# Performance work log

Measured on AMD Instinct MI355X. Metric: run time of the kernel, lower is better.

## Reference

```python
import jax, jax.numpy as jnp
import numpy as np
import math

D_MODEL = 1024
NHEAD = 16
D_HEAD = D_MODEL // NHEAD
TAU = 300.0
DELTA = 5.0 * 60.0  # delta_minutes -> seconds


def setup_inputs() -> dict:
    key = jax.random.key(0)
    ks = jax.random.split(key, 10)
    B, M = 4, 2048
    H = jax.random.normal(ks[0], (B, M, D_MODEL), dtype=jnp.float32)
    patch_mask = jax.random.randint(ks[1], (B, M), 0, 2).astype(jnp.int32)
    s = 1.0 / math.sqrt(D_MODEL)
    Wq = jax.random.normal(ks[2], (D_MODEL, D_MODEL), dtype=jnp.float32) * s
    bq = jnp.zeros((D_MODEL,), dtype=jnp.float32)
    Wk = jax.random.normal(ks[3], (D_MODEL, D_MODEL), dtype=jnp.float32) * s
    bk = jnp.zeros((D_MODEL,), dtype=jnp.float32)
    Wv = jax.random.normal(ks[4], (D_MODEL, D_MODEL), dtype=jnp.float32) * s
    bv = jnp.zeros((D_MODEL,), dtype=jnp.float32)
    Wo = jax.random.normal(ks[5], (D_MODEL, D_MODEL), dtype=jnp.float32) * s
    bo = jnp.zeros((D_MODEL,), dtype=jnp.float32)
    return {"H": H, "patch_mask": patch_mask, "Wq": Wq, "bq": bq,
            "Wk": Wk, "bk": bk, "Wv": Wv, "bv": bv, "Wo": Wo, "bo": bo}


def _time_bias(M):
    idx = jnp.arange(M)
    dist = jnp.abs(idx[:, None] - idx[None, :]).astype(jnp.float32) * DELTA
    w = jnp.exp(-dist / max(TAU, 1e-6))
    return jnp.log(w + 1e-12)  # (M, M)


def reference(H, patch_mask, Wq, bq, Wk, bk, Wv, bv, Wo, bo):
    B, M, D = H.shape
    nh, dh = NHEAD, D_HEAD
    # projections -> (B, nh, M, dh)
    q = (H @ Wq.T + bq).reshape(B, M, nh, dh).transpose(0, 2, 1, 3)
    k = (H @ Wk.T + bk).reshape(B, M, nh, dh).transpose(0, 2, 1, 3)
    v = (H @ Wv.T + bv).reshape(B, M, nh, dh).transpose(0, 2, 1, 3)
    attn = jnp.einsum('bhqd,bhkd->bhqk', q, k) / math.sqrt(dh)
    attn = attn + _time_bias(M)[None, None, :, :]
    key_pad = patch_mask <= 0  # (B, M)
    attn = jnp.where(key_pad[:, None, None, :], -1e9, attn)
    A = jax.nn.softmax(attn, axis=-1)
    out = jnp.einsum('bhqk,bhkd->bhqd', A, v)
    out = out.transpose(0, 2, 1, 3).reshape(B, M, D)
    out = out @ Wo.T + bo
    out = out * patch_mask[:, :, None].astype(out.dtype)
    return out
```

## Files before the change

kernel.cpp:

```cpp
#include <hip/hip_runtime.h>
#include <stdint.h>

typedef short short8 __attribute__((ext_vector_type(8)));
typedef float f32x4 __attribute__((ext_vector_type(4)));

#define B_    4
#define M_    2048
#define D_    1024
#define NH_   16
#define DH_   64
#define LOG2E 1.44269504f

__device__ __forceinline__ short f2bf(float f) {
  union { float f; uint32_t u; } v; v.f = f;
  uint32_t r = (v.u + 0x7fffu + ((v.u >> 16) & 1u)) >> 16;
  return (short)r;
}

__device__ __forceinline__ void gl_lds16(const void* g, void* l) {
  __builtin_amdgcn_global_load_lds(
      (__attribute__((address_space(1))) void*)(g),
      (__attribute__((address_space(3))) void*)(l),
      16, 0, 0);
}

__device__ __forceinline__ f32x4 mfma16(short8 a, short8 b, f32x4 c) {
  return __builtin_amdgcn_mfma_f32_16x16x32_bf16(a, b, c, 0, 0, 0);
}

__global__ __launch_bounds__(256) void cvt_all(const float* __restrict__ H,
                                               const float* __restrict__ s0,
                                               const float* __restrict__ s1,
                                               const float* __restrict__ s2,
                                               const float* __restrict__ s3,
                                               short* __restrict__ dH,
                                               short* __restrict__ d0,
                                               short* __restrict__ d1,
                                               short* __restrict__ d2,
                                               short* __restrict__ d3) {
  const int bidx = blockIdx.x;
  const float* src;
  short* dst;
  int i;
  if (bidx < 8192) {
    src = H; dst = dH; i = bidx * 256 + threadIdx.x;
  } else {
    const int y = (bidx - 8192) >> 10;
    src = (y == 0) ? s0 : (y == 1) ? s1 : (y == 2) ? s2 : s3;
    dst = (y == 0) ? d0 : (y == 1) ? d1 : (y == 2) ? d2 : d3;
    i = ((bidx - 8192) & 1023) * 256 + threadIdx.x;
  }
  float4 v = ((const float4*)src)[i];
  short4 o;
  o.x = f2bf(v.x); o.y = f2bf(v.y); o.z = f2bf(v.z); o.w = f2bf(v.w);
  ((short4*)dst)[i] = o;
}

__global__ __launch_bounds__(256, 3) void gemm_qkv(const short* __restrict__ A,
                                                   const short* __restrict__ Wqb,
                                                   const short* __restrict__ Wkb,
                                                   const short* __restrict__ Wvb,
                                                   const float* __restrict__ bq,
                                                   const float* __restrict__ bk,
                                                   const float* __restrict__ bv,
                                                   short* __restrict__ Qo,
                                                   short* __restrict__ Ko,
                                                   short* __restrict__ Vo) {
  __shared__ char smem_raw[34816];
  short* Abuf = (short*)smem_raw;
  short* Bbuf = (short*)smem_raw + 4096;

  const int L = blockIdx.x + 8 * (blockIdx.y + 64 * blockIdx.z);
  const int xcd = L & 7;
  const int s = L >> 3;
  const int m_local = s & 7;
  const int nz = s >> 3;
  const int nt = nz & 7, z = nz >> 3;
  const int m0 = (xcd * 8 + m_local) * 128;
  const int n0 = nt * 128;

  const short* Bt = (z == 0) ? Wqb : (z == 1) ? Wkb : Wvb;
  const float* bias = (z == 0) ? bq : (z == 1) ? bk : bv;
  const float scale = (z == 0) ? 0.125f : 1.0f;

  const int tid = threadIdx.x;
  const int w = tid >> 6, l = tid & 63;
  const int q4 = l >> 4, c = l & 15;
  const int wr = w >> 1, wc = w & 1;

  f32x4 acc[4][4] = {};
  const int arow = (l >> 2);
  const int acol = (l & 3) * 8;

  for (int kk = 0; kk < 32; ++kk) {
    const int k0 = kk * 32;
#pragma unroll
    for (int st = 0; st < 2; ++st) {
      const int chunk = w * 2 + st;
      gl_lds16(A + (size_t)(m0 + chunk * 16 + arow) * 1024 + k0 + acol,
               Abuf + chunk * 512);
      gl_lds16(Bt + (size_t)(n0 + chunk * 16 + arow) * 1024 + k0 + acol,
               Bbuf + chunk * 512);
    }
    __syncthreads();
    short8 af[4], bfr[4];
#pragma unroll
    for (int i = 0; i < 4; ++i)
      af[i] = *(const short8*)(Abuf + (wr * 64 + i * 16 + c) * 32 + q4 * 8);
#pragma unroll
    for (int j = 0; j < 4; ++j)
      bfr[j] = *(const short8*)(Bbuf + (wc * 64 + j * 16 + c) * 32 + q4 * 8);
#pragma unroll
    for (int i = 0; i < 4; ++i)
#pragma unroll
      for (int j = 0; j < 4; ++j)
        acc[i][j] = mfma16(af[i], bfr[j], acc[i][j]);
    __syncthreads();
  }

  if (z < 2) {
    short* Cb = (short*)smem_raw;
    short* out = (z == 0) ? Qo : Ko;
#pragma unroll
    for (int j = 0; j < 4; ++j) {
      const float bvv = bias[n0 + wc * 64 + j * 16 + c];
#pragma unroll
      for (int i = 0; i < 4; ++i)
#pragma unroll
        for (int r = 0; r < 4; ++r)
          Cb[(wr * 64 + i * 16 + q4 * 4 + r) * 136 + wc * 64 + j * 16 + c] =
              f2bf((acc[i][j][r] + bvv) * scale);
    }
    __syncthreads();
#pragma unroll
    for (int p = 0; p < 8; ++p) {
      const int g = p * 256 + tid;
      const int row = g >> 4, seg = g & 15;
      *(short8*)(out + (size_t)(m0 + row) * 1024 + n0 + seg * 8) =
          *(const short8*)(Cb + row * 136 + seg * 8);
    }
  } else {
    short* Cb = (short*)smem_raw;
#pragma unroll
    for (int j = 0; j < 4; ++j) {
      const float bvv = bias[n0 + wc * 64 + j * 16 + c];
#pragma unroll
      for (int i = 0; i < 4; ++i) {
        short4 pk;
        pk.x = f2bf(acc[i][j][0] + bvv);
        pk.y = f2bf(acc[i][j][1] + bvv);
        pk.z = f2bf(acc[i][j][2] + bvv);
        pk.w = f2bf(acc[i][j][3] + bvv);
        *(short4*)(Cb + (wc * 64 + j * 16 + c) * 136 + wr * 64 + i * 16 + q4 * 4) = pk;
      }
    }
    __syncthreads();
    const int bb = m0 >> 11;
    const int tokb = m0 & 2047;
#pragma unroll
    for (int p = 0; p < 8; ++p) {
      const int g = p * 256 + tid;
      const int col = g >> 4, rseg = g & 15;
      const int colg = n0 + col;
      const int hh = colg >> 6, dd = colg & 63;
      *(short8*)(Vo + ((size_t)(bb * NH_ + hh) * DH_ + dd) * M_ + tokb + rseg * 8) =
          *(const short8*)(Cb + col * 136 + rseg * 8);
    }
  }
}

__global__ __launch_bounds__(256) void gemm_oproj(const short* __restrict__ A,
                                                  const short* __restrict__ Bt,
                                                  const float* __restrict__ bias,
                                                  const int* __restrict__ pmask,
                                                  float* __restrict__ outp) {
  __shared__ char smem[17408];
  short* Abuf = (short*)smem;
  short* Bbuf = (short*)(smem + 8192);

  const int L = blockIdx.x + 16 * blockIdx.y;
  const int xcd = L & 7;
  const int s = L >> 3;
  const int m_local = s & 7;
  const int nt = s >> 3;
  const int m0 = (xcd * 8 + m_local) * 128;
  const int n0 = nt * 64;

  const int tid = threadIdx.x;
  const int w = tid >> 6, l = tid & 63;
  const int q4 = l >> 4, c = l & 15;
  const int wr = w >> 1, wc = w & 1;

  f32x4 acc[4][2] = {};
  const int arow = (l >> 2);
  const int acol = (l & 3) * 8;

  for (int kk = 0; kk < 32; ++kk) {
    const int k0 = kk * 32;
#pragma unroll
    for (int st = 0; st < 2; ++st) {
      const int chunk = w * 2 + st;
      gl_lds16(A + (size_t)(m0 + chunk * 16 + arow) * 1024 + k0 + acol,
               Abuf + chunk * 512);
    }
    gl_lds16(Bt + (size_t)(n0 + w * 16 + arow) * 1024 + k0 + acol,
             Bbuf + w * 512);
    __syncthreads();
    short8 af[4], bfr[2];
#pragma unroll
    for (int i = 0; i < 4; ++i)
      af[i] = *(const short8*)(Abuf + (wr * 64 + i * 16 + c) * 32 + q4 * 8);
#pragma unroll
    for (int j = 0; j < 2; ++j)
      bfr[j] = *(const short8*)(Bbuf + (wc * 32 + j * 16 + c) * 32 + q4 * 8);
#pragma unroll
    for (int i = 0; i < 4; ++i)
#pragma unroll
      for (int j = 0; j < 2; ++j)
        acc[i][j] = mfma16(af[i], bfr[j], acc[i][j]);
    __syncthreads();
  }

  float* Cf = (float*)smem;
#pragma unroll
  for (int half = 0; half < 2; ++half) {
    __syncthreads();
    if (wr == half) {
#pragma unroll
      for (int j = 0; j < 2; ++j) {
        const float bvv = bias[n0 + wc * 32 + j * 16 + c];
#pragma unroll
        for (int i = 0; i < 4; ++i)
#pragma unroll
          for (int r = 0; r < 4; ++r)
            Cf[(i * 16 + q4 * 4 + r) * 68 + wc * 32 + j * 16 + c] =
                acc[i][j][r] + bvv;
      }
    }
    __syncthreads();
#pragma unroll
    for (int p = 0; p < 4; ++p) {
      const int g = p * 256 + tid;
      const int row = g >> 4, seg = g & 15;
      const int rowg = m0 + half * 64 + row;
      const float mmv = (pmask[rowg] > 0) ? 1.0f : 0.0f;
      float4 v = *(const float4*)(Cf + row * 68 + seg * 4);
      v.x *= mmv; v.y *= mmv; v.z *= mmv; v.w *= mmv;
      *(float4*)(outp + (size_t)rowg * 1024 + n0 + seg * 4) = v;
    }
  }
}

__global__ __launch_bounds__(256) void attn_kernel(const short* __restrict__ Qb,
                                                   const short* __restrict__ Kb,
                                                   const short* __restrict__ Vtb,
                                                   const int* __restrict__ pmask,
                                                   short* __restrict__ Attb) {
  __shared__ char smem[20480];
  short* Ks0 = (short*)smem;
  short* Ks1 = (short*)(smem + 4096);
  short* Vs0 = (short*)(smem + 8192);
  short* Vs1 = (short*)(smem + 12288);
  short* Ps  = (short*)(smem + 16384);

  const int tid = threadIdx.x;
  const int w = tid >> 6, l = tid & 63;
  const int q4 = l >> 4, c = l & 15;
  const int qt = blockIdx.x, h = blockIdx.y, b = blockIdx.z;
  const short* Qrow = Qb + (size_t)(b * M_) * D_ + h * DH_;
  const short* Kbase = Kb + (size_t)(b * M_) * D_ + h * DH_;
  const short* Vbase = Vtb + (size_t)(b * NH_ + h) * DH_ * M_;
  const int qrow0 = qt * 64 + w * 16;

  short8 aq0 = *(const short8*)(Qrow + (size_t)(qrow0 + c) * D_ + q4 * 8);
  short8 aq1 = *(const short8*)(Qrow + (size_t)(qrow0 + c) * D_ + 32 + q4 * 8);

  const int jt0 = max(0, 2 * qt - 2);
  const int jt1 = min(M_ / 32 - 1, 2 * qt + 3);

  const int kh = tid >> 7, krow = (tid >> 2) & 31, ch = tid & 3;
  const int vrow = tid >> 2;

  {
    const int j0 = jt0 * 32;
    gl_lds16(Kbase + (size_t)(j0 + krow) * D_ + kh * 32 + ch * 8, (char*)Ks0 + tid * 16);
    gl_lds16(Vbase + (size_t)vrow * M_ + j0 + ch * 8, (char*)Vs0 + tid * 16);
  }
  __syncthreads();

  f32x4 o[4] = {};
  float lrun[4] = {0.f, 0.f, 0.f, 0.f};
  short* Pw = Ps + w * 512;

  for (int jt = jt0; jt <= jt1; ++jt) {
    const int buf = (jt - jt0) & 1;
    const int j0 = jt * 32;
    if (jt < jt1) {
      const int j0n = j0 + 32;
      gl_lds16(Kbase + (size_t)(j0n + krow) * D_ + kh * 32 + ch * 8,
               (char*)(buf ? Ks0 : Ks1) + tid * 16);
      gl_lds16(Vbase + (size_t)vrow * M_ + j0n + ch * 8,
               (char*)(buf ? Vs0 : Vs1) + tid * 16);
    }
    const short* Kt = buf ? Ks1 : Ks0;
    const short* Vt = buf ? Vs1 : Vs0;
    short8 b00 = *(const short8*)(Kt + c * 32 + q4 * 8);
    short8 b10 = *(const short8*)(Kt + 1024 + c * 32 + q4 * 8);
    short8 b01 = *(const short8*)(Kt + (16 + c) * 32 + q4 * 8);
    short8 b11 = *(const short8*)(Kt + 1024 + (16 + c) * 32 + q4 * 8);
    f32x4 s0 = {}, s1 = {};
    s0 = mfma16(aq0, b00, s0);
    s0 = mfma16(aq1, b10, s0);
    s1 = mfma16(aq0, b01, s1);
    s1 = mfma16(aq1, b11, s1);

    const float w0m = (pmask[b * M_ + j0 + c] > 0) ? 1.f : 0.f;
    const float w1m = (pmask[b * M_ + j0 + 16 + c] > 0) ? 1.f : 0.f;

#pragma unroll
    for (int r = 0; r < 4; ++r) {
      const int qr = qrow0 + q4 * 4 + r;
      const float d0 = fminf(fabsf((float)(qr - (j0 + c))), 28.0f);
      const float d1 = fminf(fabsf((float)(qr - (j0 + 16 + c))), 28.0f);
      const float p0 = exp2f((s0[r] - d0) * LOG2E) * w0m;
      const float p1 = exp2f((s1[r] - d1) * LOG2E) * w1m;
      Pw[(q4 * 4 + r) * 32 + c] = f2bf(p0);
      Pw[(q4 * 4 + r) * 32 + 16 + c] = f2bf(p1);
      lrun[r] += p0 + p1;
    }
    short8 pa = *(const short8*)(Pw + c * 32 + q4 * 8);
#pragma unroll
    for (int f = 0; f < 4; ++f) {
      short8 bv = *(const short8*)(Vt + (f * 16 + c) * 32 + q4 * 8);
      o[f] = mfma16(pa, bv, o[f]);
    }
    __syncthreads();
  }

#pragma unroll
  for (int r = 0; r < 4; ++r) {
#pragma unroll
    for (int off = 1; off < 16; off <<= 1)
      lrun[r] += __shfl_xor(lrun[r], off);
  }

  short* Cb = (short*)smem;
#pragma unroll
  for (int r = 0; r < 4; ++r) {
    const float inv = 1.0f / lrun[r];
#pragma unroll
    for (int f = 0; f < 4; ++f)
      Cb[(w * 16 + q4 * 4 + r) * 72 + f * 16 + c] = f2bf(o[f][r] * inv);
  }
  __syncthreads();
#pragma unroll
  for (int p = 0; p < 2; ++p) {
    const int u = p * 256 + tid;
    const int row = u >> 3, seg = u & 7;
    *(short8*)(Attb + (size_t)(b * M_ + qt * 64 + row) * D_ + h * DH_ + seg * 8) =
        *(const short8*)(Cb + row * 72 + seg * 8);
  }
}

extern "C" void kernel_launch(void* const* d_in, const int* in_sizes, int n_in,
                              void* d_out, int out_size, void* d_ws, size_t ws_size,
                              hipStream_t stream) {
  const float* H     = (const float*)d_in[0];
  const int*   pmask = (const int*)d_in[1];
  const float* Wq    = (const float*)d_in[2];
  const float* bq    = (const float*)d_in[3];
  const float* Wk    = (const float*)d_in[4];
  const float* bk    = (const float*)d_in[5];
  const float* Wv    = (const float*)d_in[6];
  const float* bv    = (const float*)d_in[7];
  const float* Wo    = (const float*)d_in[8];
  const float* bo    = (const float*)d_in[9];
  float* out = (float*)d_out;
  char* ws = (char*)d_ws;

  short* Hb   = (short*)(ws);
  short* Attb = (short*)(ws);
  short* Wqb  = (short*)(ws + (16u << 20));
  short* Wkb  = (short*)(ws + (18u << 20));
  short* Wvb  = (short*)(ws + (20u << 20));
  short* Wob  = (short*)(ws + (22u << 20));
  short* Qb   = (short*)(ws + (24u << 20));
  short* Kb2  = (short*)(ws + (40u << 20));
  short* Vtb  = (short*)(ws + (56u << 20));

  cvt_all<<<8192 + 4096, 256, 0, stream>>>(H, Wq, Wk, Wv, Wo,
                                           Hb, Wqb, Wkb, Wvb, Wob);

  dim3 gq(8, 64, 3);
  gemm_qkv<<<gq, 256, 0, stream>>>(Hb, Wqb, Wkb, Wvb, bq, bk, bv, Qb, Kb2, Vtb);

  attn_kernel<<<dim3(M_ / 64, NH_, B_), 256, 0, stream>>>(Qb, Kb2, Vtb, pmask, Attb);

  gemm_oproj<<<dim3(16, 64), 256, 0, stream>>>(Attb, Wob, bo, pmask, out);
}
```

Baseline: 222.1 us.

## Double-buffer LDS tiles in QKV and output-projection GEMMs

Both GEMM kernels now use two LDS buffers for the A and B tiles. The next k-slice is loaded with global_load_lds while the MFMAs run on the current slice, and the tile for the first iteration is loaded before the loop. This aims to hide global-memory latency behind matrix compute instead of stalling on load then barrier each iteration. The cost is more LDS in the output-projection kernel, which may lower occupancy, and correctness relies on the trailing barrier waiting for the async loads to finish.

Result: no change. 221.4 us (-0.3%).

```diff
diff --git a/kernel.cpp b/kernel.cpp
--- a/kernel.cpp
+++ b/kernel.cpp
@@ -67,8 +67,10 @@
                                                    short* __restrict__ Ko,
                                                    short* __restrict__ Vo) {
   __shared__ char smem_raw[34816];
-  short* Abuf = (short*)smem_raw;
-  short* Bbuf = (short*)smem_raw + 4096;
+  short* Ab0 = (short*)smem_raw;
+  short* Ab1 = (short*)(smem_raw + 8192);
+  short* Bb0 = (short*)(smem_raw + 16384);
+  short* Bb1 = (short*)(smem_raw + 24576);
 
   const int L = blockIdx.x + 8 * (blockIdx.y + 64 * blockIdx.z);
   const int xcd = L & 7;
@@ -92,24 +94,36 @@
   const int arow = (l >> 2);
   const int acol = (l & 3) * 8;
 
+#pragma unroll
+  for (int st = 0; st < 2; ++st) {
+    const int chunk = w * 2 + st;
+    gl_lds16(A + (size_t)(m0 + chunk * 16 + arow) * 1024 + acol, Ab0 + chunk * 512);
+    gl_lds16(Bt + (size_t)(n0 + chunk * 16 + arow) * 1024 + acol, Bb0 + chunk * 512);
+  }
+  __syncthreads();
+
   for (int kk = 0; kk < 32; ++kk) {
-    const int k0 = kk * 32;
-#pragma unroll
-    for (int st = 0; st < 2; ++st) {
-      const int chunk = w * 2 + st;
-      gl_lds16(A + (size_t)(m0 + chunk * 16 + arow) * 1024 + k0 + acol,
-               Abuf + chunk * 512);
-      gl_lds16(Bt + (size_t)(n0 + chunk * 16 + arow) * 1024 + k0 + acol,
-               Bbuf + chunk * 512);
-    }
-    __syncthreads();
+    const int cur = kk & 1;
+    if (kk + 1 < 32) {
+      const int k0n = (kk + 1) * 32;
+#pragma unroll
+      for (int st = 0; st < 2; ++st) {
+        const int chunk = w * 2 + st;
+        gl_lds16(A + (size_t)(m0 + chunk * 16 + arow) * 1024 + k0n + acol,
+                 (cur ? Ab0 : Ab1) + chunk * 512);
+        gl_lds16(Bt + (size_t)(n0 + chunk * 16 + arow) * 1024 + k0n + acol,
+                 (cur ? Bb0 : Bb1) + chunk * 512);
+      }
+    }
+    const short* Ab = cur ? Ab1 : Ab0;
+    const short* Bb = cur ? Bb1 : Bb0;
     short8 af[4], bfr[4];
 #pragma unroll
     for (int i = 0; i < 4; ++i)
-      af[i] = *(const short8*)(Abuf + (wr * 64 + i * 16 + c) * 32 + q4 * 8);
+      af[i] = *(const short8*)(Ab + (wr * 64 + i * 16 + c) * 32 + q4 * 8);
 #pragma unroll
     for (int j = 0; j < 4; ++j)
-      bfr[j] = *(const short8*)(Bbuf + (wc * 64 + j * 16 + c) * 32 + q4 * 8);
+      bfr[j] = *(const short8*)(Bb + (wc * 64 + j * 16 + c) * 32 + q4 * 8);
 #pragma unroll
     for (int i = 0; i < 4; ++i)
 #pragma unroll
@@ -174,9 +188,11 @@
                                                   const float* __restrict__ bias,
                                                   const int* __restrict__ pmask,
                                                   float* __restrict__ outp) {
-  __shared__ char smem[17408];
-  short* Abuf = (short*)smem;
-  short* Bbuf = (short*)(smem + 8192);
+  __shared__ char smem[24576];
+  short* Ab0 = (short*)smem;
+  short* Ab1 = (short*)(smem + 8192);
+  short* Bb0 = (short*)(smem + 16384);
+  short* Bb1 = (short*)(smem + 20480);
 
   const int L = blockIdx.x + 16 * blockIdx.y;
   const int xcd = L & 7;
@@ -195,24 +211,36 @@
   const int arow = (l >> 2);
   const int acol = (l & 3) * 8;
 
+#pragma unroll
+  for (int st = 0; st < 2; ++st) {
+    const int chunk = w * 2 + st;
+    gl_lds16(A + (size_t)(m0 + chunk * 16 + arow) * 1024 + acol, Ab0 + chunk * 512);
+  }
+  gl_lds16(Bt + (size_t)(n0 + w * 16 + arow) * 1024 + acol, Bb0 + w * 512);
+  __syncthreads();
+
   for (int kk = 0; kk < 32; ++kk) {
-    const int k0 = kk * 32;
-#pragma unroll
-    for (int st = 0; st < 2; ++st) {
-      const int chunk = w * 2 + st;
-      gl_lds16(A + (size_t)(m0 + chunk * 16 + arow) * 1024 + k0 + acol,
-               Abuf + chunk * 512);
-    }
-    gl_lds16(Bt + (size_t)(n0 + w * 16 + arow) * 1024 + k0 + acol,
-             Bbuf + w * 512);
-    __syncthreads();
+    const int cur = kk & 1;
+    if (kk + 1 < 32) {
+      const int k0n = (kk + 1) * 32;
+#pragma unroll
+      for (int st = 0; st < 2; ++st) {
+        const int chunk = w * 2 + st;
+        gl_lds16(A + (size_t)(m0 + chunk * 16 + arow) * 1024 + k0n + acol,
+                 (cur ? Ab0 : Ab1) + chunk * 512);
+      }
+      gl_lds16(Bt + (size_t)(n0 + w * 16 + arow) * 1024 + k0n + acol,
+               (cur ? Bb0 : Bb1) + w * 512);
+    }
+    const short* Ab = cur ? Ab1 : Ab0;
+    const short* Bb = cur ? Bb1 : Bb0;
     short8 af[4], bfr[2];
 #pragma unroll
     for (int i = 0; i < 4; ++i)
-      af[i] = *(const short8*)(Abuf + (wr * 64 + i * 16 + c) * 32 + q4 * 8);
+      af[i] = *(const short8*)(Ab + (wr * 64 + i * 16 + c) * 32 + q4 * 8);
 #pragma unroll
     for (int j = 0; j < 2; ++j)
-      bfr[j] = *(const short8*)(Bbuf + (wc * 32 + j * 16 + c) * 32 + q4 * 8);
+      bfr[j] = *(const short8*)(Bb + (wc * 32 + j * 16 + c) * 32 + q4 * 8);
 #pragma unroll
     for (int i = 0; i < 4; ++i)
 #pragma unroll
```
